# Performance work log

Hardware: AMD Instinct MI355X
Metric: run time of the kernel (lower is better)

The kernel has to match this reference:

```python
import jax, jax.numpy as jnp
from jax import lax
import numpy as np

N, C, H, W = 8, 256, 96, 96
K = 5            # d_conv=4 forced odd -> 5 in FauxScan1D
HID = 2 * C      # ff_mult * dim


def setup_inputs() -> dict:
    key = jax.random.key(0)
    ks = iter(jax.random.split(key, 40))
    nrm = lambda *s: jax.random.normal(next(ks), s, jnp.float32) * 0.02
    inp = {'x': jax.random.normal(next(ks), (N, C, H, W), jnp.float32)}
    inp['ln1_w'] = jnp.ones((C,), jnp.float32)
    inp['ln1_b'] = jnp.zeros((C,), jnp.float32)
    inp['dw_w'] = nrm(3, 3, 1, C)   # depthwise 3x3, HWIO with feature_group_count=C
    inp['dw_b'] = jnp.zeros((C,), jnp.float32)
    for d in ('lr', 'rl', 'tb', 'bt'):
        inp[d + '_dw_w'] = nrm(K, 1, C)   # depthwise conv1d, WIO
        inp[d + '_dw_b'] = jnp.zeros((C,), jnp.float32)
        inp[d + '_g_w'] = nrm(C, C)       # 1x1 gate conv (out, in)
        inp[d + '_g_b'] = jnp.zeros((C,), jnp.float32)
    inp['fuse_w'] = nrm(C, C)
    inp['fuse_b'] = jnp.zeros((C,), jnp.float32)
    inp['ln2_w'] = jnp.ones((C,), jnp.float32)
    inp['ln2_b'] = jnp.zeros((C,), jnp.float32)
    inp['ff1_w'] = nrm(2 * HID, C)
    inp['ff1_b'] = jnp.zeros((2 * HID,), jnp.float32)
    inp['ff2_w'] = nrm(C, HID)
    inp['ff2_b'] = jnp.zeros((C,), jnp.float32)
    return inp


def _ln2d(x, w, b, eps=1e-6):
    # LayerNorm2d: per-(sample, channel) stats over H,W
    m = x.mean(axis=(2, 3), keepdims=True)
    v = ((x - m) ** 2).mean(axis=(2, 3), keepdims=True)
    return (x - m) * lax.rsqrt(v + eps) * w[None, :, None, None] + b[None, :, None, None]


def _scan1d(seq, dw_w, dw_b, g_w, g_b):
    # FauxScan1D: seq (B, L, C) -> dwconv1d(k=5, pad=2) * sigmoid(pointwise gate)
    c = seq.shape[-1]
    y = lax.conv_general_dilated(seq, dw_w, (1,), [(K // 2, K // 2)],
                                 dimension_numbers=('NWC', 'WIO', 'NWC'),
                                 feature_group_count=c) + dw_b
    g = jax.nn.sigmoid(jnp.einsum('blc,dc->bld', seq, g_w) + g_b)
    return y * g


def _forward(x, ln1_w, ln1_b, dw_w, dw_b,
             lr_dw_w, lr_dw_b, lr_g_w, lr_g_b,
             rl_dw_w, rl_dw_b, rl_g_w, rl_g_b,
             tb_dw_w, tb_dw_b, tb_g_w, tb_g_b,
             bt_dw_w, bt_dw_b, bt_g_w, bt_g_b,
             fuse_w, fuse_b, ln2_w, ln2_b, ff1_w, ff1_b, ff2_w, ff2_b):
    n, c, hh, ww = x.shape
    y = _ln2d(x, ln1_w, ln1_b)
    y = lax.conv_general_dilated(y, dw_w, (1, 1), [(1, 1), (1, 1)],
                                 dimension_numbers=('NCHW', 'HWIO', 'NCHW'),
                                 feature_group_count=c) + dw_b[None, :, None, None]
    y = jnp.transpose(y, (0, 2, 3, 1))  # NHWC
    # lr: rows as sequences
    o = _scan1d(y.reshape(n * hh, ww, c), lr_dw_w, lr_dw_b, lr_g_w, lr_g_b).reshape(n, hh, ww, c)
    # rl: flip width, scan, flip back
    yf = jnp.flip(y, 2).reshape(n * hh, ww, c)
    o = o + jnp.flip(_scan1d(yf, rl_dw_w, rl_dw_b, rl_g_w, rl_g_b).reshape(n, hh, ww, c), 2)
    # tb: columns as sequences
    yt = jnp.transpose(y, (0, 2, 1, 3)).reshape(n * ww, hh, c)
    o = o + jnp.transpose(_scan1d(yt, tb_dw_w, tb_dw_b, tb_g_w, tb_g_b).reshape(n, ww, hh, c), (0, 2, 1, 3))
    # bt: flip height, columns, scan, undo
    yb = jnp.transpose(jnp.flip(y, 1), (0, 2, 1, 3)).reshape(n * ww, hh, c)
    o = o + jnp.flip(jnp.transpose(_scan1d(yb, bt_dw_w, bt_dw_b, bt_g_w, bt_g_b).reshape(n, ww, hh, c), (0, 2, 1, 3)), 1)
    y = jnp.transpose(o, (0, 3, 1, 2))  # back to NCHW
    y = jnp.einsum('nchw,dc->ndhw', y, fuse_w) + fuse_b[None, :, None, None]
    x = x + y
    z = _ln2d(x, ln2_w, ln2_b)
    z = jnp.einsum('nchw,dc->ndhw', z, ff1_w) + ff1_b[None, :, None, None]
    a, g = jnp.split(z, 2, axis=1)  # GLU on channel dim
    z = a * jax.nn.sigmoid(g)
    z = jnp.einsum('nchw,dc->ndhw', z, ff2_w) + ff2_b[None, :, None, None]
    return x + z


def reference(x, ln1_w, ln1_b, dw_w, dw_b,
              lr_dw_w, lr_dw_b, lr_g_w, lr_g_b,
              rl_dw_w, rl_dw_b, rl_g_w, rl_g_b,
              tb_dw_w, tb_dw_b, tb_g_w, tb_g_b,
              bt_dw_w, bt_dw_b, bt_g_w, bt_g_b,
              fuse_w, fuse_b, ln2_w, ln2_b, ff1_w, ff1_b, ff2_w, ff2_b):
    return _forward(x, ln1_w, ln1_b, dw_w, dw_b,
                    lr_dw_w, lr_dw_b, lr_g_w, lr_g_b,
                    rl_dw_w, rl_dw_b, rl_g_w, rl_g_b,
                    tb_dw_w, tb_dw_b, tb_g_w, tb_g_b,
                    bt_dw_w, bt_dw_b, bt_g_w, bt_g_b,
                    fuse_w, fuse_b, ln2_w, ln2_b, ff1_w, ff1_b, ff2_w, ff2_b)
```

## Files before the change

### kernel.cpp

```cpp
#include <hip/hip_runtime.h>

#define TPB 256
#define HWSZ 9216

typedef __attribute__((ext_vector_type(8))) short short8x;
typedef __attribute__((ext_vector_type(4))) float f32x4;
typedef unsigned short ushort_t;
typedef unsigned int uint_t;

__device__ __forceinline__ float sigf(float v) { return 1.0f / (1.0f + __expf(-v)); }

__device__ __forceinline__ ushort_t f2bf(float f) {
  uint_t u = __float_as_uint(f);
  u = (u + 0x7fffu + ((u >> 16) & 1u)) >> 16;
  return (ushort_t)u;
}
__device__ __forceinline__ float bf2f(ushort_t h) {
  return __uint_as_float(((uint_t)h) << 16);
}

__device__ __forceinline__ int swz32(int p, int c) {
  return p * 1024 + ((((c * 4) ^ ((p & 7) << 4)) ^ (((p >> 3) & 3) << 2)));
}

__global__ __launch_bounds__(TPB) void k_pack(
    const float* __restrict__ lrg, const float* __restrict__ rlg,
    const float* __restrict__ tbg, const float* __restrict__ btg,
    const float* __restrict__ fusew, const float* __restrict__ ff1w,
    const float* __restrict__ ff2w,
    ushort_t* __restrict__ Gp, ushort_t* __restrict__ Ftp,
    ushort_t* __restrict__ W1p, ushort_t* __restrict__ W2p) {
  int i = blockIdx.x * TPB + threadIdx.x;
  if (i < 262144) {
    int d = i >> 16, r = i & 65535;
    int kt = r >> 13, nt = (r >> 9) & 15, l = (r >> 3) & 63, j = r & 7;
    int k = kt * 32 + (l >> 4) * 8 + j;
    int n_ = nt * 16 + (l & 15);
    const float* g = (d == 0) ? lrg : (d == 1) ? rlg : (d == 2) ? tbg : btg;
    Gp[i] = f2bf(g[n_ * 256 + k]);
  } else if (i < 327680) {
    int r = i - 262144;
    int kt = r >> 13, nt = (r >> 9) & 15, l = (r >> 3) & 63, j = r & 7;
    int k = kt * 32 + (l >> 4) * 8 + j;
    int n_ = nt * 16 + (l & 15);
    Ftp[r] = f2bf(fusew[n_ * 256 + k]);
  } else if (i < 589824) {
    int r = i - 327680;
    int kt = r >> 15, pb = (r >> 10) & 31, ag = (r >> 9) & 1;
    int l = (r >> 3) & 63, j = r & 7;
    int k = kt * 32 + (l >> 4) * 8 + j;
    int colb = pb * 16 + (l & 15);
    int col = ag ? (512 + colb) : colb;
    W1p[r] = f2bf(ff1w[col * 256 + k]);
  } else if (i < 720896) {
    int r = i - 589824;
    int kt = r >> 13, nt = (r >> 9) & 15, l = (r >> 3) & 63, j = r & 7;
    int k = kt * 32 + (l >> 4) * 8 + j;
    int n_ = nt * 16 + (l & 15);
    W2p[r] = f2bf(ff2w[n_ * 512 + k]);
  }
}

__global__ __launch_bounds__(TPB) void k_stats(const float* __restrict__ src,
                                               float* __restrict__ mean,
                                               float* __restrict__ rstd) {
  int nc = blockIdx.x;
  const float4* p = (const float4*)(src + (long)nc * HWSZ);
  float s = 0.f, s2 = 0.f;
  for (int i = threadIdx.x; i < 2304; i += TPB) {
    float4 v = p[i];
    s += (v.x + v.y) + (v.z + v.w);
    s2 = fmaf(v.x, v.x, fmaf(v.y, v.y, fmaf(v.z, v.z, fmaf(v.w, v.w, s2))));
  }
#pragma unroll
  for (int off = 32; off > 0; off >>= 1) {
    s += __shfl_down(s, off);
    s2 += __shfl_down(s2, off);
  }
  __shared__ float ls[4], ls2[4];
  int lane = threadIdx.x & 63, wv = threadIdx.x >> 6;
  if (lane == 0) { ls[wv] = s; ls2[wv] = s2; }
  __syncthreads();
  if (threadIdx.x == 0) {
    float S = ls[0] + ls[1] + ls[2] + ls[3];
    float S2 = ls2[0] + ls2[1] + ls2[2] + ls2[3];
    float m = S * (1.0f / HWSZ);
    float var = S2 * (1.0f / HWSZ) - m * m;
    mean[nc] = m;
    rstd[nc] = rsqrtf(fmaxf(var, 0.f) + 1e-6f);
  }
}

__global__ __launch_bounds__(TPB) void k_lndw(
    const float* __restrict__ x, const float* __restrict__ mean1,
    const float* __restrict__ rstd1, const float* __restrict__ ln1w,
    const float* __restrict__ ln1b, const float* __restrict__ dww,
    const float* __restrict__ dwb, ushort_t* __restrict__ y,
    ushort_t* __restrict__ yT) {
  __shared__ __align__(16) ushort_t xs[6 * 32 * 104];
  __shared__ __align__(16) ushort_t ot[2 * 96 * 32];
  __shared__ float sc[32], sh[32];

  int tid = threadIdx.x;
  int bid = blockIdx.x;
  int cb = (bid & 7) * 32;
  int hb = (bid >> 3) % 24;
  int n  = bid / 192;
  int h0 = hb * 4;

  if (tid < 32) {
    int c = cb + tid;
    int nc = n * 256 + c;
    float scale = rstd1[nc] * ln1w[c];
    sc[tid] = scale;
    sh[tid] = ln1b[c] - mean1[nc] * scale;
  }
  if (tid < 192) {
    xs[tid * 104 + 3] = 0;
    xs[tid * 104 + 100] = 0;
  }
  __syncthreads();

  for (int i = tid; i < 4608; i += TPB) {
    int rc = i / 24;
    int f4 = i - rc * 24;
    int row = rc >> 5, c = rc & 31;
    int hh = h0 - 1 + row;
    uint2 pk = make_uint2(0, 0);
    if (hh >= 0 && hh < 96) {
      float4 v = *(const float4*)(x + (long)(n * 256 + cb + c) * HWSZ +
                                  hh * 96 + f4 * 4);
      float scale = sc[c], shift = sh[c];
      ushort_t p0 = f2bf(fmaf(v.x, scale, shift));
      ushort_t p1 = f2bf(fmaf(v.y, scale, shift));
      ushort_t p2 = f2bf(fmaf(v.z, scale, shift));
      ushort_t p3 = f2bf(fmaf(v.w, scale, shift));
      pk.x = (uint_t)p0 | ((uint_t)p1 << 16);
      pk.y = (uint_t)p2 | ((uint_t)p3 << 16);
    }
    *(uint2*)(xs + rc * 104 + 4 + f4 * 4) = pk;
  }
  __syncthreads();

  int c = tid & 31, grp = tid >> 5;
  int w0 = grp * 12;
  float wgt[9];
#pragma unroll
  for (int t = 0; t < 9; ++t) wgt[t] = dww[t * 256 + cb + c];
  float bias = dwb[cb + c];

#pragma unroll
  for (int half = 0; half < 2; ++half) {
    float vals[2][12];
#pragma unroll
    for (int sub = 0; sub < 2; ++sub) {
      int orow = half * 2 + sub;
      float R[3][14];
#pragma unroll
      for (int rr = 0; rr < 3; ++rr) {
        const ushort_t* p = xs + ((orow + rr) * 32 + c) * 104;
        R[rr][0] = bf2f(p[3 + w0]);
        ushort4 q0 = *(const ushort4*)(p + 4 + w0);
        ushort4 q1 = *(const ushort4*)(p + 8 + w0);
        ushort4 q2 = *(const ushort4*)(p + 12 + w0);
        R[rr][1] = bf2f(q0.x);  R[rr][2] = bf2f(q0.y);
        R[rr][3] = bf2f(q0.z);  R[rr][4] = bf2f(q0.w);
        R[rr][5] = bf2f(q1.x);  R[rr][6] = bf2f(q1.y);
        R[rr][7] = bf2f(q1.z);  R[rr][8] = bf2f(q1.w);
        R[rr][9] = bf2f(q2.x);  R[rr][10] = bf2f(q2.y);
        R[rr][11] = bf2f(q2.z); R[rr][12] = bf2f(q2.w);
        R[rr][13] = bf2f(p[16 + w0]);
      }
#pragma unroll
      for (int k = 0; k < 12; ++k) {
        float acc = bias;
#pragma unroll
        for (int rr = 0; rr < 3; ++rr) {
          acc = fmaf(R[rr][k], wgt[rr * 3 + 0], acc);
          acc = fmaf(R[rr][k + 1], wgt[rr * 3 + 1], acc);
          acc = fmaf(R[rr][k + 2], wgt[rr * 3 + 2], acc);
        }
        vals[sub][k] = acc;
      }
    }
    if (half == 1) __syncthreads();
#pragma unroll
    for (int sub = 0; sub < 2; ++sub)
#pragma unroll
      for (int k = 0; k < 12; ++k)
        ot[(sub * 96 + w0 + k) * 32 + c] = f2bf(vals[sub][k]);
    __syncthreads();
#pragma unroll
    for (int it = 0; it < 3; ++it) {
      int u = it * 256 + tid;
      int r2 = (u >= 384) ? 1 : 0;
      int rem = u - r2 * 384;
      int w = rem >> 2, cq = rem & 3;
      uint4 v = *(const uint4*)(ot + (r2 * 96 + w) * 32 + cq * 8);
      int h = h0 + half * 2 + r2;
      *(uint4*)(y + ((long)(n * 96 + h) * 96 + w) * 256 + cb + cq * 8) = v;
      *(uint4*)(yT + ((long)(n * 96 + w) * 96 + h) * 256 + cb + cq * 8) = v;
    }
  }
}

__global__ __launch_bounds__(512, 4) void k_scan(
    const ushort_t* __restrict__ src, const uint4* __restrict__ gp4,
    const float* __restrict__ dwaw, const float* __restrict__ dwab,
    const float* __restrict__ gab, const float* __restrict__ dwbw,
    const float* __restrict__ dwbb, const float* __restrict__ gbb,
    ushort_t* __restrict__ dst) {
  __shared__ __align__(16) char pool[34816];
  char* ylds = pool;
  char* olds = pool + 26624;

  int tid = threadIdx.x;
  int bid = blockIdx.x;
  int seg = bid & 1, line = (bid >> 1) % 96, n = bid / 192;
  int p0 = seg * 48;
  long lbase = (long)(n * 96 + line) * 96;

  for (int u = tid; u < 52 * 32; u += 512) {
    int r = u >> 5, ks = u & 31;
    int q = p0 - 2 + r;
    uint4 v = make_uint4(0, 0, 0, 0);
    if (q >= 0 && q < 96)
      v = *(const uint4*)(src + (lbase + q) * 256 + ks * 8);
    *(uint4*)(ylds + r * 512 + ((ks * 16) ^ ((r & 7) << 4))) = v;
  }
  __syncthreads();

  int l = tid & 63, w = tid >> 6;
  int llo = l & 15, lhi = l >> 4;

  float part[3][2][4];

#pragma unroll
  for (int diri = 0; diri < 2; ++diri) {
    f32x4 acc[3][2];
#pragma unroll
    for (int mf = 0; mf < 3; ++mf)
#pragma unroll
      for (int ntl = 0; ntl < 2; ++ntl) acc[mf][ntl] = (f32x4){0.f, 0.f, 0.f, 0.f};

    const uint4* gbase = gp4 + ((long)(diri * 8) * 16 + w * 2) * 64 + l;
    short8x bc0 = *(const short8x*)(gbase);
    short8x bc1 = *(const short8x*)(gbase + 64);
#pragma unroll
    for (int kt = 0; kt < 8; ++kt) {
      short8x bn0, bn1;
      if (kt < 7) {
        bn0 = *(const short8x*)(gbase + (kt + 1) * 1024);
        bn1 = *(const short8x*)(gbase + (kt + 1) * 1024 + 64);
      }
      short8x a[3];
#pragma unroll
      for (int mf = 0; mf < 3; ++mf) {
        int arow = 2 + mf * 16 + llo;
        a[mf] = *(const short8x*)(ylds + arow * 512 +
                                  ((kt * 64 + lhi * 16) ^ ((arow & 7) << 4)));
      }
#pragma unroll
      for (int mf = 0; mf < 3; ++mf) {
        acc[mf][0] = __builtin_amdgcn_mfma_f32_16x16x32_bf16(a[mf], bc0, acc[mf][0], 0, 0, 0);
        acc[mf][1] = __builtin_amdgcn_mfma_f32_16x16x32_bf16(a[mf], bc1, acc[mf][1], 0, 0, 0);
      }
      bc0 = bn0;
      bc1 = bn1;
    }

    const float* dwv = diri ? dwbw : dwaw;
    const float* dbv = diri ? dwbb : dwab;
    const float* gbv = diri ? gbb : gab;
#pragma unroll
    for (int ntl = 0; ntl < 2; ++ntl) {
      int c = (w * 2 + ntl) * 16 + llo;
      float wt[5];
#pragma unroll
      for (int t = 0; t < 5; ++t)
        wt[t] = diri ? dwv[(4 - t) * 256 + c] : dwv[t * 256 + c];
      float cb = dbv[c], gb = gbv[c];
#pragma unroll
      for (int mf = 0; mf < 3; ++mf) {
        int pbase = mf * 16 + lhi * 4;
        float yv[8];
#pragma unroll
        for (int t = 0; t < 8; ++t) {
          int ry = pbase + t;
          yv[t] = bf2f(*(const ushort_t*)(ylds + ry * 512 +
                                          ((c * 2) ^ ((ry & 7) << 4))));
        }
#pragma unroll
        for (int r = 0; r < 4; ++r) {
          float conv = cb;
#pragma unroll
          for (int t = 0; t < 5; ++t) conv = fmaf(yv[r + t], wt[t], conv);
          float val = conv * sigf(acc[mf][ntl][r] + gb);
          if (diri == 0) part[mf][ntl][r] = val;
          else           part[mf][ntl][r] += val;
        }
      }
    }
  }

#pragma unroll
  for (int mf = 0; mf < 3; ++mf) {
    __syncthreads();
#pragma unroll
    for (int ntl = 0; ntl < 2; ++ntl) {
      int c = (w * 2 + ntl) * 16 + llo;
#pragma unroll
      for (int r = 0; r < 4; ++r) {
        int p = lhi * 4 + r;
        *(ushort_t*)(olds + p * 512 + ((c * 2) ^ ((p & 7) << 4))) =
            f2bf(part[mf][ntl][r]);
      }
    }
    __syncthreads();
    {
      int p = tid >> 5, ks = tid & 31;
      uint4 v = *(const uint4*)(olds + p * 512 + ((ks * 16) ^ ((p & 7) << 4)));
      *(uint4*)(dst + (lbase + p0 + mf * 16 + p) * 256 + ks * 8) = v;
    }
  }
}

__global__ __launch_bounds__(512, 4) void k_fuse(
    const ushort_t* __restrict__ o, const ushort_t* __restrict__ oT,
    const ushort_t* __restrict__ Ftp, const float* __restrict__ fuseb,
    const float* __restrict__ x, float* __restrict__ out) {
  __shared__ __align__(16) char pool[24576];

  int tid = threadIdx.x;
  int pix0 = blockIdx.x * 48;
  int n = pix0 / HWSZ, hw0 = pix0 % HWSZ;
  int h = hw0 / 96, w0 = hw0 % 96;

  for (int u = tid; u < 48 * 32; u += 512) {
    int r = u >> 5, ks = u & 31;
    uint4 va = *(const uint4*)(o + (long)(pix0 + r) * 256 + ks * 8);
    uint4 vb = *(const uint4*)(oT + ((long)(n * 96 + w0 + r) * 96 + h) * 256 + ks * 8);
    ushort_t* a8 = (ushort_t*)&va;
    ushort_t* b8 = (ushort_t*)&vb;
#pragma unroll
    for (int j = 0; j < 8; ++j) a8[j] = f2bf(bf2f(a8[j]) + bf2f(b8[j]));
    *(uint4*)(pool + r * 512 + ((ks * 16) ^ ((r & 7) << 4))) = va;
  }
  __syncthreads();

  int l = tid & 63, w = tid >> 6;
  int llo = l & 15, lhi = l >> 4;

  const uint4* fp4 = (const uint4*)Ftp;
  f32x4 acc[3][2];
#pragma unroll
  for (int mf = 0; mf < 3; ++mf)
#pragma unroll
    for (int ntl = 0; ntl < 2; ++ntl) acc[mf][ntl] = (f32x4){0.f, 0.f, 0.f, 0.f};

  const uint4* fbase = fp4 + (long)(w * 2) * 64 + l;
  short8x bc0 = *(const short8x*)(fbase);
  short8x bc1 = *(const short8x*)(fbase + 64);
#pragma unroll
  for (int kt = 0; kt < 8; ++kt) {
    short8x bn0, bn1;
    if (kt < 7) {
      bn0 = *(const short8x*)(fbase + (kt + 1) * 1024);
      bn1 = *(const short8x*)(fbase + (kt + 1) * 1024 + 64);
    }
    short8x a[3];
#pragma unroll
    for (int mf = 0; mf < 3; ++mf) {
      int arow = mf * 16 + llo;
      a[mf] = *(const short8x*)(pool + arow * 512 +
                                ((kt * 64 + lhi * 16) ^ ((arow & 7) << 4)));
    }
#pragma unroll
    for (int mf = 0; mf < 3; ++mf) {
      acc[mf][0] = __builtin_amdgcn_mfma_f32_16x16x32_bf16(a[mf], bc0, acc[mf][0], 0, 0, 0);
      acc[mf][1] = __builtin_amdgcn_mfma_f32_16x16x32_bf16(a[mf], bc1, acc[mf][1], 0, 0, 0);
    }
    bc0 = bn0;
    bc1 = bn1;
  }

#pragma unroll
  for (int mf = 0; mf < 3; ++mf) {
    __syncthreads();
#pragma unroll
    for (int ntl = 0; ntl < 2; ++ntl) {
      int c = (w * 2 + ntl) * 16 + llo;
      float fb = fuseb[c];
#pragma unroll
      for (int r = 0; r < 4; ++r) {
        int p = lhi * 4 + r;
        *(float*)(pool + swz32(p, c)) = acc[mf][ntl][r] + fb;
      }
    }
    __syncthreads();
    for (int i = tid; i < 4096; i += 512) {
      int c = i >> 4, p = i & 15;
      long addr = (long)(n * 256 + c) * HWSZ + hw0 + mf * 16 + p;
      out[addr] = x[addr] + *(const float*)(pool + swz32(p, c));
    }
  }
}

__global__ __launch_bounds__(512, 4) void k_ff1(
    const float* __restrict__ xres, const float* __restrict__ mean2,
    const float* __restrict__ rstd2, const float* __restrict__ ln2w,
    const float* __restrict__ ln2b, const ushort_t* __restrict__ W1p,
    const float* __restrict__ ff1b, ushort_t* __restrict__ u) {
  __shared__ char hA[96 * 512];
  __shared__ float sc[256], sh[256];

  int tid = threadIdx.x;
  int pix0 = blockIdx.x * 96;
  int n = pix0 / HWSZ, hw0 = pix0 % HWSZ;

  if (tid < 256) {
    int nc = n * 256 + tid;
    float scale = rstd2[nc] * ln2w[tid];
    sc[tid] = scale;
    sh[tid] = ln2b[tid] - mean2[nc] * scale;
  }
  __syncthreads();

  for (int i = tid; i < 6144; i += 512) {
    int cp = i / 48, pp = i % 48;
    int c0 = cp * 2;
    long base0 = (long)(n * 256 + c0) * HWSZ + hw0 + pp * 2;
    float2 v0 = *(const float2*)(xres + base0);
    float2 v1 = *(const float2*)(xres + base0 + HWSZ);
    float s0 = sc[c0], h0 = sh[c0];
    float s1 = sc[c0 + 1], h1 = sh[c0 + 1];
    int p0 = pp * 2;
    uint_t w0 = (uint_t)f2bf(fmaf(v0.x, s0, h0)) |
                ((uint_t)f2bf(fmaf(v1.x, s1, h1)) << 16);
    uint_t w1 = (uint_t)f2bf(fmaf(v0.y, s0, h0)) |
                ((uint_t)f2bf(fmaf(v1.y, s1, h1)) << 16);
    *(uint_t*)(hA + p0 * 512 + ((c0 * 2) ^ ((p0 & 7) << 4))) = w0;
    *(uint_t*)(hA + (p0 + 1) * 512 + ((c0 * 2) ^ (((p0 + 1) & 7) << 4))) = w1;
  }
  __syncthreads();

  int l = tid & 63, w = tid >> 6;
  int llo = l & 15, lhi = l >> 4;

  const uint4* W1p4 = (const uint4*)W1p;
#pragma unroll
  for (int q = 0; q < 4; ++q) {
    int pb = q * 8 + w;
    f32x4 ca[6][2];
#pragma unroll
    for (int mf = 0; mf < 6; ++mf) {
      ca[mf][0] = (f32x4){0.f, 0.f, 0.f, 0.f};
      ca[mf][1] = (f32x4){0.f, 0.f, 0.f, 0.f};
    }
    const uint4* wb = W1p4 + (long)(pb * 2) * 64 + l;
    short8x bca = *(const short8x*)(wb);
    short8x bcg = *(const short8x*)(wb + 64);
#pragma unroll
    for (int kt = 0; kt < 8; ++kt) {
      short8x bna, bng;
      if (kt < 7) {
        bna = *(const short8x*)(wb + (kt + 1) * 4096);
        bng = *(const short8x*)(wb + (kt + 1) * 4096 + 64);
      }
      short8x a[6];
#pragma unroll
      for (int mf = 0; mf < 6; ++mf) {
        int arow = mf * 16 + llo;
        a[mf] = *(const short8x*)(hA + arow * 512 +
                                  ((kt * 64 + lhi * 16) ^ ((arow & 7) << 4)));
      }
#pragma unroll
      for (int mf = 0; mf < 6; ++mf) {
        ca[mf][0] = __builtin_amdgcn_mfma_f32_16x16x32_bf16(a[mf], bca, ca[mf][0], 0, 0, 0);
        ca[mf][1] = __builtin_amdgcn_mfma_f32_16x16x32_bf16(a[mf], bcg, ca[mf][1], 0, 0, 0);
      }
      bca = bna;
      bcg = bng;
    }
    int ucol = pb * 16 + llo;
    float ba = ff1b[ucol], bg = ff1b[512 + ucol];
    int rb0 = (pix0 >> 2) + lhi;
#pragma unroll
    for (int mf = 0; mf < 6; ++mf) {
      ushort_t b0 = f2bf((ca[mf][0][0] + ba) * sigf(ca[mf][1][0] + bg));
      ushort_t b1 = f2bf((ca[mf][0][1] + ba) * sigf(ca[mf][1][1] + bg));
      ushort_t b2 = f2bf((ca[mf][0][2] + ba) * sigf(ca[mf][1][2] + bg));
      ushort_t b3 = f2bf((ca[mf][0][3] + ba) * sigf(ca[mf][1][3] + bg));
      uint2 pk;
      pk.x = (uint_t)b0 | ((uint_t)b1 << 16);
      pk.y = (uint_t)b2 | ((uint_t)b3 << 16);
      *(uint2*)(u + ((long)(rb0 + mf * 4) * 512 + ucol) * 4) = pk;
    }
  }
}

__global__ __launch_bounds__(512, 4) void k_ff2(
    const ushort_t* __restrict__ u, const ushort_t* __restrict__ W2p,
    const float* __restrict__ ff2b, float* __restrict__ out) {
  __shared__ __align__(16) char pool[24576];

  int tid = threadIdx.x;
  int pix0 = blockIdx.x * 96;
  int n = pix0 / HWSZ, hw0 = pix0 % HWSZ;
  int rb0 = pix0 >> 2;

  int l = tid & 63, w = tid >> 6;
  int llo = l & 15, lhi = l >> 4;

  const uint4* W2p4 = (const uint4*)W2p;

  f32x4 zacc[6][2];
#pragma unroll
  for (int mf = 0; mf < 6; ++mf) {
    zacc[mf][0] = (f32x4){0.f, 0.f, 0.f, 0.f};
    zacc[mf][1] = (f32x4){0.f, 0.f, 0.f, 0.f};
  }

#pragma unroll
  for (int kc = 0; kc < 4; ++kc) {
    __syncthreads();
    for (int i = tid; i < 3072; i += 512) {
      int col = i & 127, rbl = i >> 7;
      uint2 v = *(const uint2*)(u + ((long)(rb0 + rbl) * 512 + kc * 128 + col) * 4);
      ushort_t* b = (ushort_t*)&v;
      int p = rbl * 4;
#pragma unroll
      for (int k = 0; k < 4; ++k)
        *(ushort_t*)(pool + (p + k) * 256 + ((col * 2) ^ (((p + k) & 7) << 4))) = b[k];
    }
    __syncthreads();
#pragma unroll
    for (int ks = 0; ks < 4; ++ks) {
      int kt = kc * 4 + ks;
      short8x a[6];
#pragma unroll
      for (int mf = 0; mf < 6; ++mf) {
        int arow = mf * 16 + llo;
        a[mf] = *(const short8x*)(pool + arow * 256 +
                                  ((ks * 64 + lhi * 16) ^ ((arow & 7) << 4)));
      }
      short8x b0 = *(const short8x*)(W2p4 + (long)(kt * 16 + w * 2) * 64 + l);
      short8x b1 = *(const short8x*)(W2p4 + (long)(kt * 16 + w * 2 + 1) * 64 + l);
#pragma unroll
      for (int mf = 0; mf < 6; ++mf) {
        zacc[mf][0] = __builtin_amdgcn_mfma_f32_16x16x32_bf16(a[mf], b0, zacc[mf][0], 0, 0, 0);
        zacc[mf][1] = __builtin_amdgcn_mfma_f32_16x16x32_bf16(a[mf], b1, zacc[mf][1], 0, 0, 0);
      }
    }
  }

#pragma unroll
  for (int mf = 0; mf < 6; ++mf) {
    __syncthreads();
#pragma unroll
    for (int ntl = 0; ntl < 2; ++ntl) {
      int c = (w * 2 + ntl) * 16 + llo;
      float fb = ff2b[c];
#pragma unroll
      for (int r = 0; r < 4; ++r) {
        int p = lhi * 4 + r;
        *(float*)(pool + swz32(p, c)) = zacc[mf][ntl][r] + fb;
      }
    }
    __syncthreads();
    for (int i = tid; i < 4096; i += 512) {
      int c = i >> 4, p = i & 15;
      long addr = (long)(n * 256 + c) * HWSZ + hw0 + mf * 16 + p;
      out[addr] += *(const float*)(pool + swz32(p, c));
    }
  }
}

extern "C" void kernel_launch(void* const* d_in, const int* in_sizes, int n_in,
                              void* d_out, int out_size, void* d_ws, size_t ws_size,
                              hipStream_t stream) {
  (void)in_sizes; (void)n_in; (void)out_size; (void)ws_size;
  const float* x     = (const float*)d_in[0];
  const float* ln1w  = (const float*)d_in[1];
  const float* ln1b  = (const float*)d_in[2];
  const float* dww   = (const float*)d_in[3];
  const float* dwb   = (const float*)d_in[4];
  const float* lr_w  = (const float*)d_in[5];
  const float* lr_b  = (const float*)d_in[6];
  const float* lr_gw = (const float*)d_in[7];
  const float* lr_gb = (const float*)d_in[8];
  const float* rl_w  = (const float*)d_in[9];
  const float* rl_b  = (const float*)d_in[10];
  const float* rl_gw = (const float*)d_in[11];
  const float* rl_gb = (const float*)d_in[12];
  const float* tb_w  = (const float*)d_in[13];
  const float* tb_b  = (const float*)d_in[14];
  const float* tb_gw = (const float*)d_in[15];
  const float* tb_gb = (const float*)d_in[16];
  const float* bt_w  = (const float*)d_in[17];
  const float* bt_b  = (const float*)d_in[18];
  const float* bt_gw = (const float*)d_in[19];
  const float* bt_gb = (const float*)d_in[20];
  const float* fusew = (const float*)d_in[21];
  const float* fuseb = (const float*)d_in[22];
  const float* ln2w  = (const float*)d_in[23];
  const float* ln2b  = (const float*)d_in[24];
  const float* ff1w  = (const float*)d_in[25];
  const float* ff1b  = (const float*)d_in[26];
  const float* ff2w  = (const float*)d_in[27];
  const float* ff2b  = (const float*)d_in[28];

  float* out = (float*)d_out;
  ushort_t* y  = (ushort_t*)d_ws;
  ushort_t* yT = y + 18874368;
  ushort_t* o  = yT + 18874368;
  ushort_t* oT = o + 18874368;
  ushort_t* uu = y;
  float* mean1 = (float*)(oT + 18874368);
  float* rstd1 = mean1 + 2048;
  float* mean2 = rstd1 + 2048;
  float* rstd2 = mean2 + 2048;
  ushort_t* Gp  = (ushort_t*)(rstd2 + 2048);
  ushort_t* Ftp = Gp + 262144;
  ushort_t* W1p = Ftp + 65536;
  ushort_t* W2p = W1p + 262144;

  k_pack<<<2816, TPB, 0, stream>>>(lr_gw, rl_gw, tb_gw, bt_gw, fusew, ff1w, ff2w,
                                   Gp, Ftp, W1p, W2p);
  k_stats<<<2048, TPB, 0, stream>>>(x, mean1, rstd1);
  k_lndw<<<1536, TPB, 0, stream>>>(x, mean1, rstd1, ln1w, ln1b, dww, dwb, y, yT);
  k_scan<<<1536, 512, 0, stream>>>(y, (const uint4*)Gp,
                                   lr_w, lr_b, lr_gb, rl_w, rl_b, rl_gb, o);
  k_scan<<<1536, 512, 0, stream>>>(yT, (const uint4*)(Gp + 131072),
                                   tb_w, tb_b, tb_gb, bt_w, bt_b, bt_gb, oT);
  k_fuse<<<1536, 512, 0, stream>>>(o, oT, Ftp, fuseb, x, out);
  k_stats<<<2048, TPB, 0, stream>>>(out, mean2, rstd2);
  k_ff1<<<768, 512, 0, stream>>>(out, mean2, rstd2, ln2w, ln2b, W1p, ff1b, uu);
  k_ff2<<<768, 512, 0, stream>>>(uu, W2p, ff2b, out);
}
```

Measured before the change: 347.0 us.

## Write GEMM epilogues directly as float4 and prefetch ff2 activation chunks into registers

The fuse and ff2 epilogues no longer stage accumulators through swizzled shared memory with two barriers per fragment. Each lane instead writes its four consecutive pixel values straight to global memory as one float4, after reading x or out. The ff2 kernel also loads the next K-chunk of u into registers while the current chunk is being multiplied, overlapping global loads with MFMA work. The trade-off is that global stores become 16-byte pieces spread across channel rows instead of fully coalesced rows, and register pressure rises from the prefetch buffer.

```diff
diff --git a/kernel.cpp b/kernel.cpp
--- a/kernel.cpp
+++ b/kernel.cpp
@@ -17,10 +17,6 @@
 }
 __device__ __forceinline__ float bf2f(ushort_t h) {
   return __uint_as_float(((uint_t)h) << 16);
-}
-
-__device__ __forceinline__ int swz32(int p, int c) {
-  return p * 1024 + ((((c * 4) ^ ((p & 7) << 4)) ^ (((p >> 3) & 3) << 2)));
 }
 
 __global__ __launch_bounds__(TPB) void k_pack(
@@ -385,25 +381,20 @@
   }
 
 #pragma unroll
-  for (int mf = 0; mf < 3; ++mf) {
-    __syncthreads();
+  for (int mf = 0; mf < 3; ++mf)
 #pragma unroll
     for (int ntl = 0; ntl < 2; ++ntl) {
       int c = (w * 2 + ntl) * 16 + llo;
       float fb = fuseb[c];
-#pragma unroll
-      for (int r = 0; r < 4; ++r) {
-        int p = lhi * 4 + r;
-        *(float*)(pool + swz32(p, c)) = acc[mf][ntl][r] + fb;
-      }
-    }
-    __syncthreads();
-    for (int i = tid; i < 4096; i += 512) {
-      int c = i >> 4, p = i & 15;
-      long addr = (long)(n * 256 + c) * HWSZ + hw0 + mf * 16 + p;
-      out[addr] = x[addr] + *(const float*)(pool + swz32(p, c));
-    }
-  }
+      long addr = (long)(n * 256 + c) * HWSZ + hw0 + mf * 16 + lhi * 4;
+      float4 xv = *(const float4*)(x + addr);
+      float4 ov;
+      ov.x = xv.x + acc[mf][ntl][0] + fb;
+      ov.y = xv.y + acc[mf][ntl][1] + fb;
+      ov.z = xv.z + acc[mf][ntl][2] + fb;
+      ov.w = xv.w + acc[mf][ntl][3] + fb;
+      *(float4*)(out + addr) = ov;
+    }
 }
 
 __global__ __launch_bounds__(512, 4) void k_ff1(
@@ -514,6 +505,14 @@
 
   const uint4* W2p4 = (const uint4*)W2p;
 
+  uint2 st[6];
+#pragma unroll
+  for (int t = 0; t < 6; ++t) {
+    int i = t * 512 + tid;
+    int col = i & 127, rbl = i >> 7;
+    st[t] = *(const uint2*)(u + ((long)(rb0 + rbl) * 512 + col) * 4);
+  }
+
   f32x4 zacc[6][2];
 #pragma unroll
   for (int mf = 0; mf < 6; ++mf) {
@@ -523,17 +522,26 @@
 
 #pragma unroll
   for (int kc = 0; kc < 4; ++kc) {
-    __syncthreads();
-    for (int i = tid; i < 3072; i += 512) {
+    if (kc) __syncthreads();
+#pragma unroll
+    for (int t = 0; t < 6; ++t) {
+      int i = t * 512 + tid;
       int col = i & 127, rbl = i >> 7;
-      uint2 v = *(const uint2*)(u + ((long)(rb0 + rbl) * 512 + kc * 128 + col) * 4);
-      ushort_t* b = (ushort_t*)&v;
       int p = rbl * 4;
+      ushort_t* b = (ushort_t*)&st[t];
 #pragma unroll
       for (int k = 0; k < 4; ++k)
         *(ushort_t*)(pool + (p + k) * 256 + ((col * 2) ^ (((p + k) & 7) << 4))) = b[k];
     }
     __syncthreads();
+    if (kc < 3) {
+#pragma unroll
+      for (int t = 0; t < 6; ++t) {
+        int i = t * 512 + tid;
+        int col = i & 127, rbl = i >> 7;
+        st[t] = *(const uint2*)(u + ((long)(rb0 + rbl) * 512 + (kc + 1) * 128 + col) * 4);
+      }
+    }
 #pragma unroll
     for (int ks = 0; ks < 4; ++ks) {
       int kt = kc * 4 + ks;
@@ -555,25 +563,19 @@
   }
 
 #pragma unroll
-  for (int mf = 0; mf < 6; ++mf) {
-    __syncthreads();
+  for (int mf = 0; mf < 6; ++mf)
 #pragma unroll
     for (int ntl = 0; ntl < 2; ++ntl) {
       int c = (w * 2 + ntl) * 16 + llo;
       float fb = ff2b[c];
-#pragma unroll
-      for (int r = 0; r < 4; ++r) {
-        int p = lhi * 4 + r;
-        *(float*)(pool + swz32(p, c)) = zacc[mf][ntl][r] + fb;
-      }
-    }
-    __syncthreads();
-    for (int i = tid; i < 4096; i += 512) {
-      int c = i >> 4, p = i & 15;
-      long addr = (long)(n * 256 + c) * HWSZ + hw0 + mf * 16 + p;
-      out[addr] += *(const float*)(pool + swz32(p, c));
-    }
-  }
+      long addr = (long)(n * 256 + c) * HWSZ + hw0 + mf * 16 + lhi * 4;
+      float4 ov = *(const float4*)(out + addr);
+      ov.x += zacc[mf][ntl][0] + fb;
+      ov.y += zacc[mf][ntl][1] + fb;
+      ov.z += zacc[mf][ntl][2] + fb;
+      ov.w += zacc[mf][ntl][3] + fb;
+      *(float4*)(out + addr) = ov;
+    }
 }
 
 extern "C" void kernel_launch(void* const* d_in, const int* in_sizes, int n_in,
```

After: 318.5 us. 1.09x faster.
